# Performance work log

Measured on AMD Instinct MI355X. Metric: run time of the kernel, lower is better.

The kernel has to match this reference:

```python
import jax, jax.numpy as jnp
import numpy as np

C = 512
B, W, H = 16, 64, 64
K = 128


def setup_inputs() -> dict:
    key = jax.random.key(0)
    ks = jax.random.split(key, 17)
    s = 0.02
    inp = {
        "x1": jax.random.normal(ks[0], (B, C, W, H), jnp.float32),
        "y1": jax.random.normal(ks[1], (B, K, C), jnp.float32),
        "x2": jax.random.normal(ks[2], (B, C, W, H), jnp.float32),
        "y2": jax.random.normal(ks[3], (B, K, C), jnp.float32),
        # 1x1 conv weights stored as [out, in]
        "wq1": jax.random.normal(ks[4], (C // 4, C), jnp.float32) * s,
        "bq1": jnp.zeros((C // 4,), jnp.float32),
        "wq2": jax.random.normal(ks[5], (C // 4, C), jnp.float32) * s,
        "bq2": jnp.zeros((C // 4,), jnp.float32),
        "wk1": jax.random.normal(ks[6], (C // 2, C), jnp.float32) * s,
        "bk1": jnp.zeros((C // 2,), jnp.float32),
        "wk2": jax.random.normal(ks[7], (C // 2, C), jnp.float32) * s,
        "bk2": jnp.zeros((C // 2,), jnp.float32),
        "wv1": jax.random.normal(ks[8], (C, C), jnp.float32) * s,
        "bv1": jnp.zeros((C,), jnp.float32),
        "wv2": jax.random.normal(ks[9], (C, C), jnp.float32) * s,
        "bv2": jnp.zeros((C,), jnp.float32),
        "scale": jnp.ones((1,), jnp.float32) * 0.5,  # nn.Parameter(zeros) would kill grads; nonzero for testing
    }
    return inp


def reference(x1, y1, x2, y2, wq1, bq1, wq2, bq2, wk1, bk1, wk2, bk2,
              wv1, bv1, wv2, bv2, scale):
    b, c, w, h = x1.shape
    n = w * h
    # 1x1 convs == channel-wise linear maps
    q1 = jnp.einsum('bcwh,dc->bdwh', x1, wq1) + bq1[None, :, None, None]
    q2 = jnp.einsum('bcwh,dc->bdwh', x2, wq2) + bq2[None, :, None, None]
    # concat along channels -> [B, C/2, N] -> [B, N, C/2]
    q = jnp.concatenate([q1, q2], axis=1).reshape(b, c // 2, n).transpose(0, 2, 1)
    k1 = y1 @ wk1.T + bk1  # [B, K, C/2]
    k2 = y2 @ wk2.T + bk2
    v1 = y1 @ wv1.T + bv1  # [B, K, C]
    v2 = y2 @ wv2.T + bv2
    e1 = jnp.einsum('bnd,bkd->bnk', q, k1)  # [B, N, K]
    e2 = jnp.einsum('bnd,bkd->bnk', q, k2)
    attn = jax.nn.softmax(jnp.abs(e1 - e2), axis=-1)
    # out = value^T @ attn^T : [B, C, N]
    o1 = jnp.einsum('bkc,bnk->bcn', v1, attn).reshape(b, c, w, h)
    o2 = jnp.einsum('bkc,bnk->bcn', v2, attn).reshape(b, c, w, h)
    out1 = scale[0] * o1 + x1
    out2 = scale[0] * o2 + x2
    return out1, out2
```

## Files before the change

### kernel.cpp

```cpp
#include <hip/hip_runtime.h>

typedef unsigned short u16;
typedef __attribute__((ext_vector_type(8))) short short8v;
typedef __attribute__((ext_vector_type(4))) float floatx4;

#define B_ 16
#define C_ 512
#define N_ 4096
#define K_ 128

__device__ __forceinline__ float bf2f(u16 u) {
    unsigned int x = ((unsigned int)u) << 16;
    return __builtin_bit_cast(float, x);
}
__device__ __forceinline__ u16 f2bf(float f) {
    unsigned int u = __builtin_bit_cast(unsigned int, f);
    u = u + 0x7FFFu + ((u >> 16) & 1u);
    return (u16)(u >> 16);
}
__device__ __forceinline__ void gload_lds16(const u16* g, u16* l) {
    __builtin_amdgcn_global_load_lds(
        (const __attribute__((address_space(1))) void*)g,
        (__attribute__((address_space(3))) void*)l, 16, 0, 0);
}

#define BARRIER_V8 do { \
    asm volatile("s_waitcnt vmcnt(8) lgkmcnt(0)" ::: "memory"); \
    __builtin_amdgcn_s_barrier(); \
    __builtin_amdgcn_sched_barrier(0); \
} while (0)
#define BARRIER_V0 do { \
    asm volatile("s_waitcnt vmcnt(0) lgkmcnt(0)" ::: "memory"); \
    __builtin_amdgcn_s_barrier(); \
    __builtin_amdgcn_sched_barrier(0); \
} while (0)

__global__ void conv_all(const float* __restrict__ y1, const float* __restrict__ y2,
                         const float* __restrict__ wk1, const float* __restrict__ wk2,
                         const float* __restrict__ wv1, const float* __restrict__ wv2,
                         const float* __restrict__ wq1, const float* __restrict__ wq2,
                         u16* y1b, u16* y2b, u16* wk1b, u16* wk2b, u16* wv1b, u16* wv2b,
                         u16* wq1t, u16* wq2t) {
    int tid = blockIdx.x * 256 + threadIdx.x;
    const int SY = B_ * K_ * C_;
    const int SWK = 256 * 512;
    const int SWV = 512 * 512;
    const int SQ = 128 * 512;
    int base = 2*SY + 2*SWK + 2*SWV;
    if (tid < base) {
        const float* src; u16* dst; int off;
        if (tid < SY)                 { src = y1;  dst = y1b;  off = tid; }
        else if (tid < 2*SY)          { src = y2;  dst = y2b;  off = tid - SY; }
        else if (tid < 2*SY+SWK)      { src = wk1; dst = wk1b; off = tid - 2*SY; }
        else if (tid < 2*SY+2*SWK)    { src = wk2; dst = wk2b; off = tid - 2*SY - SWK; }
        else if (tid < 2*SY+2*SWK+SWV){ src = wv1; dst = wv1b; off = tid - 2*SY - 2*SWK; }
        else                          { src = wv2; dst = wv2b; off = tid - 2*SY - 2*SWK - SWV; }
        dst[off] = f2bf(src[off]);
    } else {
        int e = tid - base;
        const float* s = (e >= SQ) ? wq2 : wq1;
        u16* d = (e >= SQ) ? wq2t : wq1t;
        e &= (SQ - 1);
        int dd = e >> 9;
        int c = e & 511;
        d[c * 128 + dd] = f2bf(s[dd * 512 + c]);
    }
}

__global__ void gemm_gkgv(const u16* __restrict__ y1b, const u16* __restrict__ y2b,
                          const u16* __restrict__ wk1b, const u16* __restrict__ wk2b,
                          const u16* __restrict__ wv1b, const u16* __restrict__ wv2b,
                          const float* __restrict__ bk1, const float* __restrict__ bk2,
                          const float* __restrict__ bv1, const float* __restrict__ bv2,
                          u16* k1b, u16* k2b, u16* vt1, u16* vt2) {
    int l = threadIdx.x;
    int id = blockIdx.x;
    const u16 *A, *Bt; const float* bias; u16* outp;
    int m0, n0, po; bool bias_m;
    if (id < 256) {
        int bx = id & 1, by = (id >> 1) & 3, z = id >> 3;
        int b = z >> 1, which = z & 1;
        A = (which ? y2b : y1b) + (size_t)b * K_ * C_;
        Bt = which ? wk2b : wk1b;
        bias = which ? bk2 : bk1;
        outp = (which ? k2b : k1b) + (size_t)b * K_ * 256;
        m0 = bx * 64; n0 = by * 64; po = 256; bias_m = false;
    } else {
        int id2 = id - 256;
        int bx = id2 & 7, by = (id2 >> 3) & 1, z = id2 >> 4;
        int b = z >> 1, which = z & 1;
        A = which ? wv2b : wv1b;
        Bt = (which ? y2b : y1b) + (size_t)b * K_ * C_;
        bias = which ? bv2 : bv1;
        outp = (which ? vt2 : vt1) + (size_t)b * C_ * K_;
        m0 = bx * 64; n0 = by * 64; po = 128; bias_m = true;
    }
    floatx4 acc[4][4] = {};
    for (int ch = 0; ch < 16; ++ch) {
        int koff = ch * 32 + (l >> 4) * 8;
        short8v a[4], wv[4];
#pragma unroll
        for (int mf = 0; mf < 4; ++mf) a[mf] = *(const short8v*)(A + (size_t)(m0 + mf*16 + (l & 15)) * 512 + koff);
#pragma unroll
        for (int nf = 0; nf < 4; ++nf) wv[nf] = *(const short8v*)(Bt + (size_t)(n0 + nf*16 + (l & 15)) * 512 + koff);
#pragma unroll
        for (int mf = 0; mf < 4; ++mf)
#pragma unroll
            for (int nf = 0; nf < 4; ++nf)
                acc[mf][nf] = __builtin_amdgcn_mfma_f32_16x16x32_bf16(a[mf], wv[nf], acc[mf][nf], 0, 0, 0);
    }
#pragma unroll
    for (int mf = 0; mf < 4; ++mf)
#pragma unroll
        for (int nf = 0; nf < 4; ++nf)
#pragma unroll
            for (int rg = 0; rg < 4; ++rg) {
                int m = m0 + mf*16 + (l >> 4)*4 + rg;
                int n = n0 + nf*16 + (l & 15);
                outp[(size_t)m * po + n] = f2bf(acc[mf][nf][rg] + (bias_m ? bias[m] : bias[n]));
            }
}

__global__ void kd_sub(const u16* __restrict__ k1b, const u16* __restrict__ k2b,
                       u16* kd) {
    int tid = blockIdx.x * 256 + threadIdx.x;
    kd[tid] = f2bf(bf2f(k1b[tid]) - bf2f(k2b[tid]));
}

__global__ void ebd_k(const u16* __restrict__ kd,
                      const float* __restrict__ bq1, const float* __restrict__ bq2,
                      float* ebd) {
    int tid = blockIdx.x * 256 + threadIdx.x;
    const u16* kb = kd + (size_t)tid * 256;
    float s = 0.f;
    for (int d = 0; d < 128; ++d) s += bq1[d] * bf2f(kb[d]);
    for (int d = 0; d < 128; ++d) s += bq2[d] * bf2f(kb[128 + d]);
    ebd[tid] = s;
}

__global__ void gemm_gkk(const u16* __restrict__ kd,
                         const u16* __restrict__ wq1t, const u16* __restrict__ wq2t,
                         u16* kkd1, u16* kkd2) {
    int l = threadIdx.x;
    int z = blockIdx.z; int b = z >> 1; int which = z & 1;
    const u16* A = kd + (size_t)b * K_ * 256 + which * 128;
    const u16* Wt = which ? wq2t : wq1t;
    u16* outp = (which ? kkd2 : kkd1) + (size_t)b * K_ * C_;
    int m0 = blockIdx.x * 64, n0 = blockIdx.y * 64;
    floatx4 acc[4][4] = {};
    for (int ch = 0; ch < 4; ++ch) {
        int koff = ch * 32 + (l >> 4) * 8;
        short8v a[4], wv[4];
#pragma unroll
        for (int mf = 0; mf < 4; ++mf) a[mf] = *(const short8v*)(A + (size_t)(m0 + mf*16 + (l & 15)) * 256 + koff);
#pragma unroll
        for (int nf = 0; nf < 4; ++nf) wv[nf] = *(const short8v*)(Wt + (size_t)(n0 + nf*16 + (l & 15)) * 128 + koff);
#pragma unroll
        for (int mf = 0; mf < 4; ++mf)
#pragma unroll
            for (int nf = 0; nf < 4; ++nf)
                acc[mf][nf] = __builtin_amdgcn_mfma_f32_16x16x32_bf16(a[mf], wv[nf], acc[mf][nf], 0, 0, 0);
    }
#pragma unroll
    for (int mf = 0; mf < 4; ++mf)
#pragma unroll
        for (int nf = 0; nf < 4; ++nf)
#pragma unroll
            for (int rg = 0; rg < 4; ++rg) {
                int m = m0 + mf*16 + (l >> 4)*4 + rg;
                int n = n0 + nf*16 + (l & 15);
                outp[(size_t)m * C_ + n] = f2bf(acc[mf][nf][rg]);
            }
}

__global__ __launch_bounds__(256, 2)
void fused_attn(const float* __restrict__ x1, const float* __restrict__ x2,
                const u16* __restrict__ kkd1, const u16* __restrict__ kkd2,
                const u16* __restrict__ vt1, const u16* __restrict__ vt2,
                const float* __restrict__ ebd, const float* __restrict__ scale_p,
                float* __restrict__ out1, float* __restrict__ out2) {
    __shared__ u16 smem[32768];
    u16* xT[2]  = { smem,         smem + 8192 };
    u16* kkS[2] = { smem + 16384, smem + 24576 };
    u16* attn_s = smem + 16384;

    int id = blockIdx.x;
    int sw = ((id & 7) << 6) | (id >> 3);
    int b = sw >> 5;
    int n0 = (sw & 31) * 128;
    int t = threadIdx.x, w = t >> 6, l = t & 63;

    const float* xs[2] = { x1 + (size_t)b * C_ * N_, x2 + (size_t)b * C_ * N_ };
    const u16* kkp[2] = { kkd1 + (size_t)b * K_ * C_, kkd2 + (size_t)b * K_ * C_ };

    floatx4 ed[2][8] = {};

    float xA0[16], xA1[16], xB0[16], xB1[16];

    auto SLOADX = [&](int s, float (&v0)[16], float (&v1)[16]) {
        int h = s >> 3, c0 = (s & 7) * 64;
        const float* xp = xs[h] + (size_t)(c0 + w * 16) * N_ + n0 + 2 * l;
#pragma unroll
        for (int j = 0; j < 16; ++j) {
            float2 f = *(const float2*)(xp + (size_t)j * N_);
            v0[j] = f.x; v1[j] = f.y;
        }
    };
    auto KLDS = [&](int s, int buf) {
        int h = s >> 3, c0 = (s & 7) * 64;
        const u16* kp = kkp[h] + c0;
#pragma unroll
        for (int i = 0; i < 4; ++i) {
            int gi = i * 256 + t;
            int key = gi >> 3, gp = gi & 7;
            gload_lds16(kp + (size_t)key * 512 + (gp ^ (key & 7)) * 8,
                        &kkS[buf][(i * 256 + w * 64) * 8]);
        }
    };
    auto SWRITEX = [&](int buf, float (&v0)[16], float (&v1)[16]) {
        short8v p00, p01, p10, p11;
#pragma unroll
        for (int j = 0; j < 8; ++j) {
            p00[j] = (short)f2bf(v0[j]);  p01[j] = (short)f2bf(v0[j + 8]);
            p10[j] = (short)f2bf(v1[j]);  p11[j] = (short)f2bf(v1[j + 8]);
        }
        u16* xb = xT[buf];
        int row0 = 2 * l, sz = l & 7;
        *(short8v*)&xb[row0 * 64 + 8 * ((w * 2) ^ sz)] = p00;
        *(short8v*)&xb[row0 * 64 + 8 * ((w * 2 + 1) ^ sz)] = p01;
        *(short8v*)&xb[(row0 + 1) * 64 + 8 * ((w * 2) ^ sz)] = p10;
        *(short8v*)&xb[(row0 + 1) * 64 + 8 * ((w * 2 + 1) ^ sz)] = p11;
    };
    auto COMPUTE = [&](int buf) {
        u16* xb = xT[buf]; u16* kb = kkS[buf];
#pragma unroll
        for (int cc = 0; cc < 2; ++cc) {
            short8v a[2];
#pragma unroll
            for (int mf = 0; mf < 2; ++mf) {
                int row = w * 32 + mf * 16 + (l & 15);
                int g = cc * 4 + (l >> 4);
                a[mf] = *(const short8v*)&xb[row * 64 + 8 * (g ^ ((row >> 1) & 7))];
            }
#pragma unroll
            for (int kf = 0; kf < 8; ++kf) {
                int key = kf * 16 + (l & 15);
                int g = cc * 4 + (l >> 4);
                short8v bb = *(const short8v*)&kb[key * 64 + 8 * (g ^ (key & 7))];
#pragma unroll
                for (int mf = 0; mf < 2; ++mf)
                    ed[mf][kf] = __builtin_amdgcn_mfma_f32_16x16x32_bf16(a[mf], bb, ed[mf][kf], 0, 0, 0);
            }
        }
    };

    SLOADX(0, xA0, xA1); KLDS(0, 0);
    SWRITEX(0, xA0, xA1);
    SLOADX(1, xB0, xB1); KLDS(1, 1);
#pragma unroll
    for (int rr = 0; rr < 8; ++rr) {
        int sA = 2 * rr, sB = 2 * rr + 1;
        BARRIER_V8;
        if (rr > 0) KLDS(sB, 1);
        COMPUTE(0);
        SWRITEX(1, xB0, xB1);
        if (sA + 2 <= 15) SLOADX(sA + 2, xA0, xA1);
        if (rr == 7) { BARRIER_V0; }
        else         { BARRIER_V8; }
        if (sA + 2 <= 15) KLDS(sA + 2, 0);
        COMPUTE(1);
        if (sB + 1 <= 15) SWRITEX(0, xA0, xA1);
        if (sB + 2 <= 15) SLOADX(sB + 2, xB0, xB1);
    }

    float ebv[8];
#pragma unroll
    for (int kf = 0; kf < 8; ++kf) ebv[kf] = ebd[b * 128 + kf * 16 + (l & 15)];
#pragma unroll
    for (int mf = 0; mf < 2; ++mf)
#pragma unroll
        for (int kf = 0; kf < 8; ++kf)
#pragma unroll
            for (int rg = 0; rg < 4; ++rg)
                ed[mf][kf][rg] = fabsf(ed[mf][kf][rg] + ebv[kf]);

    float mx[2][4], sm[2][4];
#pragma unroll
    for (int mf = 0; mf < 2; ++mf)
#pragma unroll
        for (int rg = 0; rg < 4; ++rg) {
            float m = fmaxf(ed[mf][0][rg], ed[mf][1][rg]);
            m = fmaxf(m, fmaxf(ed[mf][2][rg], ed[mf][3][rg]));
            m = fmaxf(m, fmaxf(ed[mf][4][rg], ed[mf][5][rg]));
            m = fmaxf(m, fmaxf(ed[mf][6][rg], ed[mf][7][rg]));
            mx[mf][rg] = m;
        }
#pragma unroll
    for (int st = 1; st < 16; st <<= 1)
#pragma unroll
        for (int mf = 0; mf < 2; ++mf)
#pragma unroll
            for (int rg = 0; rg < 4; ++rg)
                mx[mf][rg] = fmaxf(mx[mf][rg], __shfl_xor(mx[mf][rg], st));
#pragma unroll
    for (int mf = 0; mf < 2; ++mf)
#pragma unroll
        for (int rg = 0; rg < 4; ++rg) sm[mf][rg] = 0.f;
#pragma unroll
    for (int mf = 0; mf < 2; ++mf)
#pragma unroll
        for (int kf = 0; kf < 8; ++kf)
#pragma unroll
            for (int rg = 0; rg < 4; ++rg) {
                float e = __expf(ed[mf][kf][rg] - mx[mf][rg]);
                ed[mf][kf][rg] = e;
                sm[mf][rg] += e;
            }
#pragma unroll
    for (int st = 1; st < 16; st <<= 1)
#pragma unroll
        for (int mf = 0; mf < 2; ++mf)
#pragma unroll
            for (int rg = 0; rg < 4; ++rg)
                sm[mf][rg] += __shfl_xor(sm[mf][rg], st);
#pragma unroll
    for (int mf = 0; mf < 2; ++mf)
#pragma unroll
        for (int rg = 0; rg < 4; ++rg) sm[mf][rg] = 1.0f / sm[mf][rg];

    __syncthreads();
#pragma unroll
    for (int mf = 0; mf < 2; ++mf)
#pragma unroll
        for (int rg = 0; rg < 4; ++rg) {
            int row = w * 32 + mf * 16 + (l >> 4) * 4 + rg;
#pragma unroll
            for (int kf = 0; kf < 8; ++kf) {
                int col = kf * 16 + (l & 15);
                attn_s[row * 128 + 8 * ((col >> 3) ^ (row & 15)) + (col & 7)] =
                    f2bf(ed[mf][kf][rg] * sm[mf][rg]);
            }
        }
    __syncthreads();

    const float sc = scale_p[0];
    const u16* vts[2] = { vt1 + (size_t)b * C_ * K_, vt2 + (size_t)b * C_ * K_ };
    float* outs[2] = { out1 + (size_t)b * C_ * N_, out2 + (size_t)b * C_ * N_ };

    short8v vfA[4], vfB[4];
    float rsA[4][8], rsB[4][8];
    auto LOADPV = [&](int s, short8v (&vf)[4], float (&rs)[4][8]) {
        int oi = s >> 3, cc = s & 7;
        const u16* vp = vts[oi] + (size_t)(cc * 64 + w * 16 + (l & 15)) * K_ + (l >> 4) * 8;
#pragma unroll
        for (int kc = 0; kc < 4; ++kc) vf[kc] = *(const short8v*)(vp + kc * 32);
        const float* rp = xs[oi] + (size_t)(cc * 64 + w * 16 + (l >> 4) * 4) * N_ + n0 + (l & 15);
#pragma unroll
        for (int rg = 0; rg < 4; ++rg)
#pragma unroll
            for (int nf = 0; nf < 8; ++nf)
                rs[rg][nf] = rp[(size_t)rg * N_ + nf * 16];
    };
    auto COMPPV = [&](int s, short8v (&vf)[4], float (&rs)[4][8]) {
        floatx4 o[8] = {};
#pragma unroll
        for (int kc = 0; kc < 4; ++kc) {
#pragma unroll
            for (int nf = 0; nf < 8; ++nf) {
                int row = nf * 16 + (l & 15);
                int g = kc * 4 + (l >> 4);
                short8v bb = *(const short8v*)&attn_s[row * 128 + 8 * (g ^ (row & 15))];
                o[nf] = __builtin_amdgcn_mfma_f32_16x16x32_bf16(vf[kc], bb, o[nf], 0, 0, 0);
            }
        }
        int oi = s >> 3, cc = s & 7;
        float* op = outs[oi];
        int cr = cc * 64 + w * 16 + (l >> 4) * 4;
#pragma unroll
        for (int rg = 0; rg < 4; ++rg) {
            size_t rowoff = (size_t)(cr + rg) * N_ + n0 + (l & 15);
#pragma unroll
            for (int nf = 0; nf < 8; ++nf)
                op[rowoff + nf * 16] = sc * o[nf][rg] + rs[rg][nf];
        }
    };

    LOADPV(0, vfA, rsA);
    LOADPV(1, vfB, rsB);
#pragma unroll
    for (int ss = 0; ss < 8; ++ss) {
        COMPPV(2 * ss, vfA, rsA);
        if (2 * ss + 2 < 16) LOADPV(2 * ss + 2, vfA, rsA);
        COMPPV(2 * ss + 1, vfB, rsB);
        if (2 * ss + 3 < 16) LOADPV(2 * ss + 3, vfB, rsB);
    }
}

extern "C" void kernel_launch(void* const* d_in, const int* in_sizes, int n_in,
                              void* d_out, int out_size, void* d_ws, size_t ws_size,
                              hipStream_t stream) {
    const float* x1 = (const float*)d_in[0];
    const float* y1 = (const float*)d_in[1];
    const float* x2 = (const float*)d_in[2];
    const float* y2 = (const float*)d_in[3];
    const float* wq1 = (const float*)d_in[4];
    const float* bq1 = (const float*)d_in[5];
    const float* wq2 = (const float*)d_in[6];
    const float* bq2 = (const float*)d_in[7];
    const float* wk1 = (const float*)d_in[8];
    const float* bk1 = (const float*)d_in[9];
    const float* wk2 = (const float*)d_in[10];
    const float* bk2 = (const float*)d_in[11];
    const float* wv1 = (const float*)d_in[12];
    const float* bv1 = (const float*)d_in[13];
    const float* wv2 = (const float*)d_in[14];
    const float* bv2 = (const float*)d_in[15];
    const float* scale = (const float*)d_in[16];

    char* ws = (char*)d_ws;
    u16* y1b  = (u16*)(ws + 0);
    u16* y2b  = (u16*)(ws + 2097152);
    u16* wk1b = (u16*)(ws + 4194304);
    u16* wk2b = (u16*)(ws + 4456448);
    u16* wv1b = (u16*)(ws + 4718592);
    u16* wv2b = (u16*)(ws + 5242880);
    u16* wq1t = (u16*)(ws + 5767168);
    u16* wq2t = (u16*)(ws + 5898240);
    u16* k1b  = (u16*)(ws + 6029312);
    u16* k2b  = (u16*)(ws + 7077888);
    u16* kd   = (u16*)(ws + 8126464);
    u16* kkd1 = (u16*)(ws + 9175040);
    u16* kkd2 = (u16*)(ws + 11272192);
    u16* vt1  = (u16*)(ws + 13369344);
    u16* vt2  = (u16*)(ws + 15466496);
    float* ebd = (float*)(ws + 17563648);

    float* out1 = (float*)d_out;
    float* out2 = out1 + (size_t)B_ * C_ * N_;

    hipLaunchKernelGGL(conv_all, dim3(11776), dim3(256), 0, stream,
                       y1, y2, wk1, wk2, wv1, wv2, wq1, wq2,
                       y1b, y2b, wk1b, wk2b, wv1b, wv2b, wq1t, wq2t);
    hipLaunchKernelGGL(gemm_gkgv, dim3(768), dim3(64), 0, stream,
                       y1b, y2b, wk1b, wk2b, wv1b, wv2b, bk1, bk2, bv1, bv2,
                       k1b, k2b, vt1, vt2);
    hipLaunchKernelGGL(kd_sub, dim3(2048), dim3(256), 0, stream, k1b, k2b, kd);
    hipLaunchKernelGGL(ebd_k, dim3(8), dim3(256), 0, stream, kd, bq1, bq2, ebd);
    hipLaunchKernelGGL(gemm_gkk, dim3(2, 8, 32), dim3(64), 0, stream,
                       kd, wq1t, wq2t, kkd1, kkd2);
    hipLaunchKernelGGL(fused_attn, dim3(512), dim3(256), 0, stream,
                       x1, x2, kkd1, kkd2, vt1, vt2, ebd, scale, out1, out2);
}
```

Baseline: 215.5 us.

## Fuse key-difference, bias-dot and Wq GEMM kernels; vectorize fp32-to-bf16 conversion

```diff
diff --git a/kernel.cpp b/kernel.cpp
--- a/kernel.cpp
+++ b/kernel.cpp
@@ -2,6 +2,7 @@
 
 typedef unsigned short u16;
 typedef __attribute__((ext_vector_type(8))) short short8v;
+typedef __attribute__((ext_vector_type(4))) unsigned short ushort4v;
 typedef __attribute__((ext_vector_type(4))) float floatx4;
 
 #define B_ 16
@@ -42,25 +43,24 @@
                          u16* y1b, u16* y2b, u16* wk1b, u16* wk2b, u16* wv1b, u16* wv2b,
                          u16* wq1t, u16* wq2t) {
     int tid = blockIdx.x * 256 + threadIdx.x;
-    const int SY = B_ * K_ * C_;
-    const int SWK = 256 * 512;
-    const int SWV = 512 * 512;
-    const int SQ = 128 * 512;
-    int base = 2*SY + 2*SWK + 2*SWV;
-    if (tid < base) {
+    const int VBASE = 720896;
+    if (tid < VBASE) {
         const float* src; u16* dst; int off;
-        if (tid < SY)                 { src = y1;  dst = y1b;  off = tid; }
-        else if (tid < 2*SY)          { src = y2;  dst = y2b;  off = tid - SY; }
-        else if (tid < 2*SY+SWK)      { src = wk1; dst = wk1b; off = tid - 2*SY; }
-        else if (tid < 2*SY+2*SWK)    { src = wk2; dst = wk2b; off = tid - 2*SY - SWK; }
-        else if (tid < 2*SY+2*SWK+SWV){ src = wv1; dst = wv1b; off = tid - 2*SY - 2*SWK; }
-        else                          { src = wv2; dst = wv2b; off = tid - 2*SY - 2*SWK - SWV; }
-        dst[off] = f2bf(src[off]);
+        if (tid < 262144)      { src = y1;  dst = y1b;  off = tid; }
+        else if (tid < 524288) { src = y2;  dst = y2b;  off = tid - 262144; }
+        else if (tid < 557056) { src = wk1; dst = wk1b; off = tid - 524288; }
+        else if (tid < 589824) { src = wk2; dst = wk2b; off = tid - 557056; }
+        else if (tid < 655360) { src = wv1; dst = wv1b; off = tid - 589824; }
+        else                   { src = wv2; dst = wv2b; off = tid - 655360; }
+        float4 v = *(const float4*)(src + (size_t)off * 4);
+        ushort4v p;
+        p[0] = f2bf(v.x); p[1] = f2bf(v.y); p[2] = f2bf(v.z); p[3] = f2bf(v.w);
+        *(ushort4v*)(dst + (size_t)off * 4) = p;
     } else {
-        int e = tid - base;
-        const float* s = (e >= SQ) ? wq2 : wq1;
-        u16* d = (e >= SQ) ? wq2t : wq1t;
-        e &= (SQ - 1);
+        int e = tid - VBASE;
+        const float* s = (e >= 65536) ? wq2 : wq1;
+        u16* d = (e >= 65536) ? wq2t : wq1t;
+        e &= 65535;
         int dd = e >> 9;
         int c = e & 511;
         d[c * 128 + dd] = f2bf(s[dd * 512 + c]);
@@ -121,38 +121,44 @@
             }
 }
 
-__global__ void kd_sub(const u16* __restrict__ k1b, const u16* __restrict__ k2b,
-                       u16* kd) {
-    int tid = blockIdx.x * 256 + threadIdx.x;
-    kd[tid] = f2bf(bf2f(k1b[tid]) - bf2f(k2b[tid]));
-}
-
-__global__ void ebd_k(const u16* __restrict__ kd,
-                      const float* __restrict__ bq1, const float* __restrict__ bq2,
-                      float* ebd) {
-    int tid = blockIdx.x * 256 + threadIdx.x;
-    const u16* kb = kd + (size_t)tid * 256;
-    float s = 0.f;
-    for (int d = 0; d < 128; ++d) s += bq1[d] * bf2f(kb[d]);
-    for (int d = 0; d < 128; ++d) s += bq2[d] * bf2f(kb[128 + d]);
-    ebd[tid] = s;
-}
-
-__global__ void gemm_gkk(const u16* __restrict__ kd,
-                         const u16* __restrict__ wq1t, const u16* __restrict__ wq2t,
-                         u16* kkd1, u16* kkd2) {
+__global__ void gemm_gkk_ebd(const u16* __restrict__ k1b, const u16* __restrict__ k2b,
+                             const u16* __restrict__ wq1t, const u16* __restrict__ wq2t,
+                             const float* __restrict__ bq1, const float* __restrict__ bq2,
+                             u16* kkd1, u16* kkd2, float* ebd) {
     int l = threadIdx.x;
-    int z = blockIdx.z; int b = z >> 1; int which = z & 1;
-    const u16* A = kd + (size_t)b * K_ * 256 + which * 128;
+    int id = blockIdx.x;
+    if (id >= 512) {
+        int tid = (id - 512) * 64 + l;
+        const u16* kb1 = k1b + (size_t)tid * 256;
+        const u16* kb2 = k2b + (size_t)tid * 256;
+        float s = 0.f;
+        for (int d = 0; d < 128; ++d) s += bq1[d] * (bf2f(kb1[d]) - bf2f(kb2[d]));
+        for (int d = 0; d < 128; ++d) s += bq2[d] * (bf2f(kb1[128 + d]) - bf2f(kb2[128 + d]));
+        ebd[tid] = s;
+        return;
+    }
+    int bx = id & 1, by = (id >> 1) & 7, z = id >> 4;
+    int b = z >> 1, which = z & 1;
+    const u16* A1 = k1b + (size_t)b * K_ * 256 + which * 128;
+    const u16* A2 = k2b + (size_t)b * K_ * 256 + which * 128;
     const u16* Wt = which ? wq2t : wq1t;
     u16* outp = (which ? kkd2 : kkd1) + (size_t)b * K_ * C_;
-    int m0 = blockIdx.x * 64, n0 = blockIdx.y * 64;
+    int m0 = bx * 64, n0 = by * 64;
     floatx4 acc[4][4] = {};
     for (int ch = 0; ch < 4; ++ch) {
         int koff = ch * 32 + (l >> 4) * 8;
         short8v a[4], wv[4];
 #pragma unroll
-        for (int mf = 0; mf < 4; ++mf) a[mf] = *(const short8v*)(A + (size_t)(m0 + mf*16 + (l & 15)) * 256 + koff);
+        for (int mf = 0; mf < 4; ++mf) {
+            size_t ro = (size_t)(m0 + mf*16 + (l & 15)) * 256 + koff;
+            short8v s1 = *(const short8v*)(A1 + ro);
+            short8v s2 = *(const short8v*)(A2 + ro);
+            short8v av;
+#pragma unroll
+            for (int j = 0; j < 8; ++j)
+                av[j] = (short)f2bf(bf2f((u16)s1[j]) - bf2f((u16)s2[j]));
+            a[mf] = av;
+        }
 #pragma unroll
         for (int nf = 0; nf < 4; ++nf) wv[nf] = *(const short8v*)(Wt + (size_t)(n0 + nf*16 + (l & 15)) * 128 + koff);
 #pragma unroll
@@ -428,7 +434,6 @@
     u16* wq2t = (u16*)(ws + 5898240);
     u16* k1b  = (u16*)(ws + 6029312);
     u16* k2b  = (u16*)(ws + 7077888);
-    u16* kd   = (u16*)(ws + 8126464);
     u16* kkd1 = (u16*)(ws + 9175040);
     u16* kkd2 = (u16*)(ws + 11272192);
     u16* vt1  = (u16*)(ws + 13369344);
@@ -438,16 +443,14 @@
     float* out1 = (float*)d_out;
     float* out2 = out1 + (size_t)B_ * C_ * N_;
 
-    hipLaunchKernelGGL(conv_all, dim3(11776), dim3(256), 0, stream,
+    hipLaunchKernelGGL(conv_all, dim3(3328), dim3(256), 0, stream,
                        y1, y2, wk1, wk2, wv1, wv2, wq1, wq2,
                        y1b, y2b, wk1b, wk2b, wv1b, wv2b, wq1t, wq2t);
     hipLaunchKernelGGL(gemm_gkgv, dim3(768), dim3(64), 0, stream,
                        y1b, y2b, wk1b, wk2b, wv1b, wv2b, bk1, bk2, bv1, bv2,
                        k1b, k2b, vt1, vt2);
-    hipLaunchKernelGGL(kd_sub, dim3(2048), dim3(256), 0, stream, k1b, k2b, kd);
-    hipLaunchKernelGGL(ebd_k, dim3(8), dim3(256), 0, stream, kd, bq1, bq2, ebd);
-    hipLaunchKernelGGL(gemm_gkk, dim3(2, 8, 32), dim3(64), 0, stream,
-                       kd, wq1t, wq2t, kkd1, kkd2);
+    hipLaunchKernelGGL(gemm_gkk_ebd, dim3(544), dim3(64), 0, stream,
+                       k1b, k2b, wq1t, wq2t, bq1, bq2, kkd1, kkd2, ebd);
     hipLaunchKernelGGL(fused_attn, dim3(512), dim3(256), 0, stream,
                        x1, x2, kkd1, kkd2, vt1, vt2, ebd, scale, out1, out2);
 }
```

New measurement: 213.2 us. About the same (-1.1%).
